# Performance work log

Measured on AMD Instinct MI355X. Metric: run time of the kernel, lower is better.

The kernel has to match this reference:

```python
import jax, jax.numpy as jnp
import numpy as np

B, S, T = 256, 2048, 64


def setup_inputs() -> dict:
    key = jax.random.key(0)
    k1, k2, k3, k4, k5 = jax.random.split(key, 5)
    emissions = jax.random.normal(k1, (B, S, T), dtype=jnp.float32)
    tags = jax.random.randint(k2, (B, S), 0, T)
    mask = jnp.ones((B, S), dtype=jnp.int32)
    start_transitions = jax.random.uniform(k3, (T,), minval=-1.0, maxval=1.0, dtype=jnp.float32)
    end_transitions = jax.random.uniform(k4, (T,), minval=-1.0, maxval=1.0, dtype=jnp.float32)
    transitions = jax.random.uniform(k5, (T, T), minval=-1.0, maxval=1.0, dtype=jnp.float32)
    return {
        'emissions': emissions,
        'start_transitions': start_transitions,
        'end_transitions': end_transitions,
        'transitions': transitions,
        'tags': tags,
        'mask': mask,
    }


def _crf_nll(emissions, start_transitions, end_transitions, transitions, tags, mask):
    # batch_first=True -> convert to time-major like the torch code
    em = jnp.swapaxes(emissions, 0, 1)            # (S, B, T)
    tg = tags.T                                   # (S, B)
    mk = mask.T.astype(emissions.dtype)           # (S, B)
    barange = jnp.arange(em.shape[1])

    # ---- numerator: score of the gold tag path ----
    score0 = start_transitions[tg[0]] + em[0, barange, tg[0]]  # (B,)

    def num_step(score, inp):
        em_i, tg_prev, tg_i, m_i = inp
        score = score + (transitions[tg_prev, tg_i] + em_i[barange, tg_i]) * m_i
        return score, None

    numerator, _ = jax.lax.scan(num_step, score0, (em[1:], tg[:-1], tg[1:], mk[1:]))
    seq_ends = mk.sum(axis=0).astype(jnp.int32) - 1            # (B,)
    last_tags = tg[seq_ends, barange]
    numerator = numerator + end_transitions[last_tags]

    # ---- denominator: log partition via forward algorithm (log-sum-exp semiring) ----
    alpha0 = start_transitions + em[0]                          # (B, T)

    def den_step(alpha, inp):
        em_i, m_i = inp
        # (B, T_prev, T_next) broadcast-add, reduce over T_prev
        nxt = jax.nn.logsumexp(alpha[:, :, None] + transitions[None, :, :] + em_i[:, None, :], axis=1)
        alpha = jnp.where(m_i[:, None] > 0, nxt, alpha)
        return alpha, None

    alpha, _ = jax.lax.scan(den_step, alpha0, (em[1:], mk[1:]))
    denominator = jax.nn.logsumexp(alpha + end_transitions, axis=1)  # (B,)

    return -(numerator - denominator).mean()


def reference(emissions, start_transitions, end_transitions, transitions, tags, mask):
    return _crf_nll(emissions, start_transitions, end_transitions, transitions, tags, mask)
```

## Files before the change

kernel.cpp:

```cpp
#include <hip/hip_runtime.h>

#define BB 256
#define SS 2048
#define TT 64
#define KC 64
#define LC 32
#define WARM 32
#define NSTEP (WARM + LC)
#define DEPTH 8
#define DEN_WAVES (BB * 4)
#define NSLOT 128
#define SLOT_STRIDE 32
#define LN2 0.69314718055994531f
#define LOG2E 1.4426950408889634f

typedef __fp16 half2v __attribute__((ext_vector_type(2)));
typedef __fp16 half8v __attribute__((ext_vector_type(8)));
typedef float float4v __attribute__((ext_vector_type(4)));

__device__ __forceinline__ float4v mfma16(half8v a, half8v b, float4v c) {
  return __builtin_amdgcn_mfma_f32_16x16x32_f16(a, b, c, 0, 0, 0);
}

#define VMW(N) asm volatile("s_waitcnt vmcnt(" #N ")" ::: "memory")

__global__ __launch_bounds__(64, 1) void crf_kernel(
    const float* __restrict__ em, const float* __restrict__ startT,
    const float* __restrict__ endT, const float* __restrict__ trans,
    const int* __restrict__ tags, const int* __restrict__ mask,
    float* __restrict__ acc, int slotmask) {
  __shared__ float lds[DEPTH * 1024];
  const int lane = threadIdx.x;

  if (blockIdx.x >= DEN_WAVES) {
    const int bb = blockIdx.x - DEN_WAVES;
    const int* tg = tags + bb * SS;
    const int* mp = mask + bb * SS;
    const float* emb = em + (size_t)bb * SS * TT;
    float part = 0.f;
    int cnt = 0;
#pragma unroll 4
    for (int k = 0; k < SS / 64; ++k) {
      int i = k * 64 + lane;
      int m = mp[i];
      cnt += m;
      if (i >= 1 && m) {
        int t1 = tg[i], t0 = tg[i - 1];
        part += trans[t0 * TT + t1] + emb[(size_t)i * TT + t1];
      }
    }
#pragma unroll
    for (int o = 32; o > 0; o >>= 1) {
      part += __shfl_xor(part, o, 64);
      cnt += __shfl_xor(cnt, o, 64);
    }
    if (lane == 0) {
      int t0 = tg[0];
      float num = part + startT[t0] + emb[t0] + endT[tg[cnt - 1]];
      atomicAdd(acc + (size_t)(blockIdx.x & slotmask) * SLOT_STRIDE,
                -num * (1.0f / BB));
    }
    return;
  }

  const int w = blockIdx.x;
  const int L = (w & 7) * (DEN_WAVES / 8) + (w >> 3);
  const int bb = L >> 2;
  const int s = lane & 15;
  const int g = lane >> 4;
  const int c = (L & 3) * 16 + s;
  const float* emB = em + (size_t)bb * SS * TT;
  const size_t rowb = (size_t)bb * SS;

  half8v A[4][2];
#pragma unroll
  for (int mt = 0; mt < 4; ++mt)
#pragma unroll
    for (int kt = 0; kt < 2; ++kt) {
      half8v f;
#pragma unroll
      for (int e = 0; e < 8; e += 2) {
        int k0 = 32 * kt + 16 * (e >> 2) + 4 * g + (e & 3);
        int m = 16 * mt + s;
        float v0 = __expf(trans[k0 * TT + m]) * 0.03125f;
        float v1 = __expf(trans[(k0 + 1) * TT + m]) * 0.03125f;
        half2v p = __builtin_amdgcn_cvt_pkrtz(v0, v1);
        f[e] = p[0];
        f[e + 1] = p[1];
      }
      A[mt][kt] = f;
    }

  half8v B0, B1;
#pragma unroll
  for (int e = 0; e < 8; ++e) {
    B0[e] = (__fp16)0.015625f;
    B1[e] = (__fp16)0.015625f;
  }
  float v_ready = 0.015625f;
  int esum = 0, nsteps = 0;
  float sS = 0.f, gamma = 0.f;
  float4v tf0, tf1, tf2, tf3;

  const int base = c * LC - WARM + 1;
  char* lbase = (char*)lds;

  auto PFS = [&](int slot, int idx) {
    int p = base + idx;
    p = p < 0 ? 0 : (p > SS - 1 ? SS - 1 : p);
    const float* r = emB + (size_t)p * TT + 4 * g;
    char* d = lbase + slot * 4096;
#pragma unroll
    for (int mt = 0; mt < 4; ++mt) {
      __builtin_amdgcn_global_load_lds(
          (const __attribute__((address_space(1))) void*)(r + 16 * mt),
          (__attribute__((address_space(3))) void*)(d + mt * 1024), 16, 0, 0);
    }
  };
  auto LDEXP = [&](int slot, float4v (&x)[4]) {
    const char* sb = lbase + slot * 4096 + lane * 16;
#pragma unroll
    for (int mt = 0; mt < 4; ++mt) x[mt] = *(const float4v*)(sb + mt * 1024);
#pragma unroll
    for (int mt = 0; mt < 4; ++mt)
#pragma unroll
      for (int e = 0; e < 4; ++e) x[mt][e] = __expf(x[mt][e]);
  };
  auto CORE = [&](const float4v (&x)[4]) {
    int eb = __builtin_bit_cast(int, v_ready) & 0x7f800000;
    float sc = __builtin_bit_cast(float, 0x7C000000 - eb);
    esum += eb >> 23;
    nsteps += 1;
    float4v xs0 = x[0] * sc, xs1 = x[1] * sc, xs2 = x[2] * sc, xs3 = x[3] * sc;
    const float4v z = {0.f, 0.f, 0.f, 0.f};
    tf0 = mfma16(A[0][0], B0, z);
    tf0 = mfma16(A[0][1], B1, tf0);
    tf1 = mfma16(A[1][0], B0, z);
    tf1 = mfma16(A[1][1], B1, tf1);
    tf2 = mfma16(A[2][0], B0, z);
    tf2 = mfma16(A[2][1], B1, tf2);
    tf3 = mfma16(A[3][0], B0, z);
    tf3 = mfma16(A[3][1], B1, tf3);
    tf0 *= xs0; tf1 *= xs1; tf2 *= xs2; tf3 *= xs3;
    v_ready = __shfl(tf0[0], s, 64);
    half2v p;
    p = __builtin_amdgcn_cvt_pkrtz(tf0[0], tf0[1]); B0[0] = p[0]; B0[1] = p[1];
    p = __builtin_amdgcn_cvt_pkrtz(tf0[2], tf0[3]); B0[2] = p[0]; B0[3] = p[1];
    p = __builtin_amdgcn_cvt_pkrtz(tf1[0], tf1[1]); B0[4] = p[0]; B0[5] = p[1];
    p = __builtin_amdgcn_cvt_pkrtz(tf1[2], tf1[3]); B0[6] = p[0]; B0[7] = p[1];
    p = __builtin_amdgcn_cvt_pkrtz(tf2[0], tf2[1]); B1[0] = p[0]; B1[1] = p[1];
    p = __builtin_amdgcn_cvt_pkrtz(tf2[2], tf2[3]); B1[2] = p[0]; B1[3] = p[1];
    p = __builtin_amdgcn_cvt_pkrtz(tf3[0], tf3[1]); B1[4] = p[0]; B1[5] = p[1];
    p = __builtin_amdgcn_cvt_pkrtz(tf3[2], tf3[3]); B1[6] = p[0]; B1[7] = p[1];
  };

#pragma unroll
  for (int k = 0; k < DEPTH; ++k) PFS(k, k);

  for (int kb = 0; kb < NSTEP - DEPTH; kb += DEPTH) {
    if (kb == WARM) {
      sS = __log2f(v_ready) + (float)(6 + esum - 116 * nsteps);
      if (c == 0) {
        float aref = startT[0] + emB[0];
        gamma = aref * LOG2E;
        sS = 0.f;
        esum = 0;
        nsteps = 0;
        v_ready = 0.015625f;
#pragma unroll
        for (int e = 0; e < 8; ++e) {
          int t0i = 16 * (e >> 2) + 4 * g + (e & 3);
          B0[e] = (__fp16)(__expf(startT[t0i] + emB[t0i] - aref) * 0.015625f);
          B1[e] = (__fp16)(__expf(startT[t0i + 32] + emB[t0i + 32] - aref) *
                           0.015625f);
        }
      }
    }
#pragma unroll
    for (int j = 0; j < DEPTH; ++j) {
      VMW(28);
      float4v x[4];
      LDEXP(j, x);
      PFS(j, kb + j + DEPTH);
      CORE(x);
    }
  }
  { VMW(28); float4v x[4]; LDEXP(0, x); CORE(x); }
  { VMW(24); float4v x[4]; LDEXP(1, x); CORE(x); }
  { VMW(20); float4v x[4]; LDEXP(2, x); CORE(x); }
  { VMW(16); float4v x[4]; LDEXP(3, x); CORE(x); }
  { VMW(12); float4v x[4]; LDEXP(4, x); CORE(x); }
  { VMW(8);  float4v x[4]; LDEXP(5, x); CORE(x); }
  { VMW(4);  float4v x[4]; LDEXP(6, x); CORE(x); }
  float qf;
  {
    half8v oB0 = B0, oB1 = B1;
    float4v o0 = tf0, o1 = tf1, o2 = tf2, o3 = tf3;
    int oes = esum, on = nsteps;
    float ov = v_ready;
    { VMW(0); float4v x[4]; LDEXP(7, x); CORE(x); }
    int p = base + (NSTEP - 1);
    int pc = p > SS - 1 ? SS - 1 : p;
    bool act = (p >= 1) && (p <= SS - 1) && (mask[rowb + pc] != 0);
    qf = act ? v_ready : ov;
    if (!act) {
      B0 = oB0; B1 = oB1; esum = oes; nsteps = on;
      tf0 = o0; tf1 = o1; tf2 = o2; tf3 = o3;
    }
  }

  float eS = __log2f(qf) + (float)(6 + esum - 116 * nsteps) + gamma;
  float contrib = LN2 * (eS - sS);

  {
    float q0l = __log2f(qf);
    float4v ar0, ar1, ar2, ar3;
    float mx = -1e30f;
#pragma unroll
    for (int r = 0; r < 4; ++r) {
      ar0[r] = LN2 * (__log2f(tf0[r]) - q0l) + endT[4 * g + r];
      ar1[r] = LN2 * (__log2f(tf1[r]) - q0l) + endT[16 + 4 * g + r];
      ar2[r] = LN2 * (__log2f(tf2[r]) - q0l) + endT[32 + 4 * g + r];
      ar3[r] = LN2 * (__log2f(tf3[r]) - q0l) + endT[48 + 4 * g + r];
      mx = fmaxf(mx, fmaxf(fmaxf(ar0[r], ar1[r]), fmaxf(ar2[r], ar3[r])));
    }
    mx = fmaxf(mx, __shfl_xor(mx, 16, 64));
    mx = fmaxf(mx, __shfl_xor(mx, 32, 64));
    float ex = 0.f;
#pragma unroll
    for (int r = 0; r < 4; ++r)
      ex += __expf(ar0[r] - mx) + __expf(ar1[r] - mx) + __expf(ar2[r] - mx) +
            __expf(ar3[r] - mx);
    ex += __shfl_xor(ex, 16, 64);
    ex += __shfl_xor(ex, 32, 64);
    if (c == KC - 1) contrib += mx + __logf(ex);
  }

  float val = (g == 0) ? contrib : 0.f;
#pragma unroll
  for (int o = 32; o > 0; o >>= 1) val += __shfl_xor(val, o, 64);
  if (lane == 0)
    atomicAdd(acc + (size_t)(blockIdx.x & slotmask) * SLOT_STRIDE,
              val * (1.0f / BB));
}

__global__ __launch_bounds__(64) void reduce_kernel(const float* __restrict__ ws,
                                                    float* __restrict__ out) {
  float v = ws[(size_t)threadIdx.x * SLOT_STRIDE] +
            ws[(size_t)(threadIdx.x + 64) * SLOT_STRIDE];
#pragma unroll
  for (int o = 32; o > 0; o >>= 1) v += __shfl_xor(v, o, 64);
  if (threadIdx.x == 0) *out = v;
}

extern "C" void kernel_launch(void* const* d_in, const int* in_sizes, int n_in,
                              void* d_out, int out_size, void* d_ws, size_t ws_size,
                              hipStream_t stream) {
  const float* em = (const float*)d_in[0];
  const float* startT = (const float*)d_in[1];
  const float* endT = (const float*)d_in[2];
  const float* trans = (const float*)d_in[3];
  const int* tags = (const int*)d_in[4];
  const int* mask = (const int*)d_in[5];
  float* out = (float*)d_out;

  const size_t need = (size_t)NSLOT * SLOT_STRIDE * sizeof(float);
  if (d_ws && ws_size >= need) {
    (void)hipMemsetAsync(d_ws, 0, need, stream);
    crf_kernel<<<DEN_WAVES + BB, 64, 0, stream>>>(em, startT, endT, trans, tags,
                                                  mask, (float*)d_ws, NSLOT - 1);
    reduce_kernel<<<1, 64, 0, stream>>>((const float*)d_ws, out);
  } else {
    (void)hipMemsetAsync(out, 0, sizeof(float), stream);
    crf_kernel<<<DEN_WAVES + BB, 64, 0, stream>>>(em, startT, endT, trans, tags,
                                                  mask, out, 0);
  }
}
```

Baseline: 259.6 us.

## Split emission loading into a producer wave and double chunk length

Each block now has two waves. A dedicated producer wave streams emission rows into a ring of LDS slots, and the compute wave consumes them after a barrier at every step. The chunk length doubles to 64 steps and the number of chunks per sequence halves to 32, so the warmup overhead per useful step falls, but the serial chain per wave gets longer. The numerator path is widened to 128 threads with an LDS reduction across the two waves. A block barrier per step adds synchronisation cost, and the removal of the old block-index swizzle changes how work is spread across CUs.

```diff
diff --git a/kernel.cpp b/kernel.cpp
--- a/kernel.cpp
+++ b/kernel.cpp
@@ -3,12 +3,12 @@
 #define BB 256
 #define SS 2048
 #define TT 64
-#define KC 64
-#define LC 32
+#define KC 32
+#define LC 64
 #define WARM 32
 #define NSTEP (WARM + LC)
 #define DEPTH 8
-#define DEN_WAVES (BB * 4)
+#define DEN_BLOCKS (BB * KC / 16)
 #define NSLOT 128
 #define SLOT_STRIDE 32
 #define LN2 0.69314718055994531f
@@ -23,25 +23,28 @@
 }
 
 #define VMW(N) asm volatile("s_waitcnt vmcnt(" #N ")" ::: "memory")
-
-__global__ __launch_bounds__(64, 1) void crf_kernel(
+#define BAR() __builtin_amdgcn_s_barrier()
+
+__global__ __launch_bounds__(128, 1) void crf_kernel(
     const float* __restrict__ em, const float* __restrict__ startT,
     const float* __restrict__ endT, const float* __restrict__ trans,
     const int* __restrict__ tags, const int* __restrict__ mask,
     float* __restrict__ acc, int slotmask) {
-  __shared__ float lds[DEPTH * 1024];
-  const int lane = threadIdx.x;
-
-  if (blockIdx.x >= DEN_WAVES) {
-    const int bb = blockIdx.x - DEN_WAVES;
+  __shared__ float lds[DEPTH * 1024 + 8];
+  const int tid = threadIdx.x;
+  const int wid = tid >> 6;
+  const int lane = tid & 63;
+
+  if (blockIdx.x >= DEN_BLOCKS) {
+    const int bb = blockIdx.x - DEN_BLOCKS;
     const int* tg = tags + bb * SS;
     const int* mp = mask + bb * SS;
     const float* emb = em + (size_t)bb * SS * TT;
     float part = 0.f;
     int cnt = 0;
 #pragma unroll 4
-    for (int k = 0; k < SS / 64; ++k) {
-      int i = k * 64 + lane;
+    for (int k = 0; k < SS / 128; ++k) {
+      int i = k * 128 + tid;
       int m = mp[i];
       cnt += m;
       if (i >= 1 && m) {
@@ -55,22 +58,59 @@
       cnt += __shfl_xor(cnt, o, 64);
     }
     if (lane == 0) {
+      lds[8192 + wid] = part;
+      lds[8194 + wid] = (float)cnt;
+    }
+    __syncthreads();
+    if (tid == 0) {
+      float pt = lds[8192] + lds[8193];
+      int ct = (int)lds[8194] + (int)lds[8195];
       int t0 = tg[0];
-      float num = part + startT[t0] + emb[t0] + endT[tg[cnt - 1]];
+      float num = pt + startT[t0] + emb[t0] + endT[tg[ct - 1]];
       atomicAdd(acc + (size_t)(blockIdx.x & slotmask) * SLOT_STRIDE,
                 -num * (1.0f / BB));
     }
     return;
   }
 
-  const int w = blockIdx.x;
-  const int L = (w & 7) * (DEN_WAVES / 8) + (w >> 3);
-  const int bb = L >> 2;
+  const int L = blockIdx.x;
+  const int bb = L >> 1;
   const int s = lane & 15;
   const int g = lane >> 4;
-  const int c = (L & 3) * 16 + s;
+  const int c = (L & 1) * 16 + s;
   const float* emB = em + (size_t)bb * SS * TT;
-  const size_t rowb = (size_t)bb * SS;
+  const int base = c * LC - WARM + 1;
+
+  if (wid == 1) {
+    char* lbase = (char*)lds;
+    auto PFS = [&](int slot, int idx) {
+      int p = base + idx;
+      p = p < 0 ? 0 : (p > SS - 1 ? SS - 1 : p);
+      const float* r = emB + (size_t)p * TT + 4 * g;
+      char* d = lbase + slot * 4096;
+#pragma unroll
+      for (int mt = 0; mt < 4; ++mt) {
+        __builtin_amdgcn_global_load_lds(
+            (const __attribute__((address_space(1))) void*)(r + 16 * mt),
+            (__attribute__((address_space(3))) void*)(d + mt * 1024), 16, 0, 0);
+      }
+    };
+#pragma unroll
+    for (int k = 0; k < DEPTH - 1; ++k) PFS(k, k);
+    for (int j = 0; j < NSTEP - 6; ++j) {
+      VMW(24);
+      BAR();
+      int sj = j + DEPTH - 1;
+      if (sj < NSTEP) PFS(sj & (DEPTH - 1), sj);
+    }
+    VMW(20); BAR();
+    VMW(16); BAR();
+    VMW(12); BAR();
+    VMW(8);  BAR();
+    VMW(4);  BAR();
+    VMW(0);  BAR();
+    return;
+  }
 
   half8v A[4][2];
 #pragma unroll
@@ -101,24 +141,10 @@
   int esum = 0, nsteps = 0;
   float sS = 0.f, gamma = 0.f;
   float4v tf0, tf1, tf2, tf3;
-
-  const int base = c * LC - WARM + 1;
-  char* lbase = (char*)lds;
-
-  auto PFS = [&](int slot, int idx) {
-    int p = base + idx;
-    p = p < 0 ? 0 : (p > SS - 1 ? SS - 1 : p);
-    const float* r = emB + (size_t)p * TT + 4 * g;
-    char* d = lbase + slot * 4096;
-#pragma unroll
-    for (int mt = 0; mt < 4; ++mt) {
-      __builtin_amdgcn_global_load_lds(
-          (const __attribute__((address_space(1))) void*)(r + 16 * mt),
-          (__attribute__((address_space(3))) void*)(d + mt * 1024), 16, 0, 0);
-    }
-  };
+  const size_t rowb = (size_t)bb * SS;
+
   auto LDEXP = [&](int slot, float4v (&x)[4]) {
-    const char* sb = lbase + slot * 4096 + lane * 16;
+    const char* sb = (const char*)lds + slot * 4096 + lane * 16;
 #pragma unroll
     for (int mt = 0; mt < 4; ++mt) x[mt] = *(const float4v*)(sb + mt * 1024);
 #pragma unroll
@@ -154,11 +180,8 @@
     p = __builtin_amdgcn_cvt_pkrtz(tf3[2], tf3[3]); B1[6] = p[0]; B1[7] = p[1];
   };
 
-#pragma unroll
-  for (int k = 0; k < DEPTH; ++k) PFS(k, k);
-
-  for (int kb = 0; kb < NSTEP - DEPTH; kb += DEPTH) {
-    if (kb == WARM) {
+  for (int j = 0; j < NSTEP - 1; ++j) {
+    if (__builtin_expect(j == WARM, 0)) {
       sS = __log2f(v_ready) + (float)(6 + esum - 116 * nsteps);
       if (c == 0) {
         float aref = startT[0] + emB[0];
@@ -176,29 +199,21 @@
         }
       }
     }
-#pragma unroll
-    for (int j = 0; j < DEPTH; ++j) {
-      VMW(28);
-      float4v x[4];
-      LDEXP(j, x);
-      PFS(j, kb + j + DEPTH);
-      CORE(x);
-    }
-  }
-  { VMW(28); float4v x[4]; LDEXP(0, x); CORE(x); }
-  { VMW(24); float4v x[4]; LDEXP(1, x); CORE(x); }
-  { VMW(20); float4v x[4]; LDEXP(2, x); CORE(x); }
-  { VMW(16); float4v x[4]; LDEXP(3, x); CORE(x); }
-  { VMW(12); float4v x[4]; LDEXP(4, x); CORE(x); }
-  { VMW(8);  float4v x[4]; LDEXP(5, x); CORE(x); }
-  { VMW(4);  float4v x[4]; LDEXP(6, x); CORE(x); }
+    BAR();
+    float4v x[4];
+    LDEXP(j & (DEPTH - 1), x);
+    CORE(x);
+  }
   float qf;
   {
     half8v oB0 = B0, oB1 = B1;
     float4v o0 = tf0, o1 = tf1, o2 = tf2, o3 = tf3;
     int oes = esum, on = nsteps;
     float ov = v_ready;
-    { VMW(0); float4v x[4]; LDEXP(7, x); CORE(x); }
+    BAR();
+    float4v x[4];
+    LDEXP((NSTEP - 1) & (DEPTH - 1), x);
+    CORE(x);
     int p = base + (NSTEP - 1);
     int pc = p > SS - 1 ? SS - 1 : p;
     bool act = (p >= 1) && (p <= SS - 1) && (mask[rowb + pc] != 0);
@@ -267,12 +282,13 @@
   const size_t need = (size_t)NSLOT * SLOT_STRIDE * sizeof(float);
   if (d_ws && ws_size >= need) {
     (void)hipMemsetAsync(d_ws, 0, need, stream);
-    crf_kernel<<<DEN_WAVES + BB, 64, 0, stream>>>(em, startT, endT, trans, tags,
-                                                  mask, (float*)d_ws, NSLOT - 1);
+    crf_kernel<<<DEN_BLOCKS + BB, 128, 0, stream>>>(em, startT, endT, trans,
+                                                    tags, mask, (float*)d_ws,
+                                                    NSLOT - 1);
     reduce_kernel<<<1, 64, 0, stream>>>((const float*)d_ws, out);
   } else {
     (void)hipMemsetAsync(out, 0, sizeof(float), stream);
-    crf_kernel<<<DEN_WAVES + BB, 64, 0, stream>>>(em, startT, endT, trans, tags,
-                                                  mask, out, 0);
-  }
-}
+    crf_kernel<<<DEN_BLOCKS + BB, 128, 0, stream>>>(em, startT, endT, trans,
+                                                    tags, mask, out, 0);
+  }
+}
```

Measured after the change: 229.3 us. 11.7% less time.
